# Performance work log

Measured on AMD Instinct MI355X. Metric: run time of the kernel, lower is better.

The kernel has to match this reference:

```python
import jax, jax.numpy as jnp
import numpy as np

EPS = 1e-4  # epsilon init kwarg


def setup_inputs() -> dict:
    key = jax.random.key(0)
    a = jax.random.normal(key, (8192, 64, 64), dtype=jnp.float32)
    # module assumes symmetric input (tf.self_adjoint_eig)
    x = 0.5 * (a + a.transpose(0, 2, 1))
    return {"x": x}


def reference(x):
    # batched symmetric eigendecomposition
    s, u = jnp.linalg.eigh(x)            # s: [b, d], u: [b, d, d]
    s = jnp.maximum(s, EPS)              # eigenvalue ReLU with shift epsilon
    # reconstruct: u @ diag(s) @ u^T
    return jnp.einsum('bik,bk,bjk->bij', u, s, u)
```

## Files before the change

### kernel.cpp

```cpp
#include <hip/hip_runtime.h>
#include <cstdint>


#define EPSV 1e-4f

typedef short bf16x8  __attribute__((ext_vector_type(8)));
typedef short short4v __attribute__((ext_vector_type(4)));
typedef float f32x16  __attribute__((ext_vector_type(16)));

__device__ __forceinline__ short f2bf(float f) {
  unsigned u = __float_as_uint(f);
  return (short)((u + 0x7FFFu + ((u >> 16) & 1u)) >> 16);
}
__device__ __forceinline__ float bf2f(short s) {
  return __uint_as_float(((unsigned)(unsigned short)s) << 16);
}
__device__ __forceinline__ int swz(int row, int byte) { return byte ^ ((row & 7) << 4); }
__device__ __forceinline__ void fence() { __asm volatile("" ::: "memory"); }

struct Frags { bf16x8 f[2][4]; };

__device__ __forceinline__ void loadFrags(const short* buf, int l31, int h, Frags& F) {
  #pragma unroll
  for (int mi = 0; mi < 2; mi++)
    #pragma unroll
    for (int ks = 0; ks < 4; ks++) {
      const int row = 32 * mi + l31;
      F.f[mi][ks] = *(const bf16x8*)((const char*)buf + swz(row, row * 128 + 32 * ks + 16 * h));
    }
}

__device__ __forceinline__ void chains3(const Frags& Ah, const Frags& Al,
                                        const Frags& Bh, const Frags& Bl,
                                        f32x16 acc[2][2]) {
  #pragma unroll
  for (int mi = 0; mi < 2; mi++)
    #pragma unroll
    for (int ni = 0; ni < 2; ni++)
      #pragma unroll
      for (int e = 0; e < 16; e++) acc[mi][ni][e] = 0.f;
#define MM(A, B) acc[mi][ni] = __builtin_amdgcn_mfma_f32_32x32x16_bf16(A, B, acc[mi][ni], 0, 0, 0)
  #pragma unroll
  for (int ks = 0; ks < 4; ks++) {
    #pragma unroll
    for (int mi = 0; mi < 2; mi++)
      #pragma unroll
      for (int ni = 0; ni < 2; ni++) MM(Ah.f[mi][ks], Bh.f[ni][ks]);
    #pragma unroll
    for (int mi = 0; mi < 2; mi++)
      #pragma unroll
      for (int ni = 0; ni < 2; ni++) MM(Ah.f[mi][ks], Bl.f[ni][ks]);
    #pragma unroll
    for (int mi = 0; mi < 2; mi++)
      #pragma unroll
      for (int ni = 0; ni < 2; ni++) MM(Al.f[mi][ks], Bh.f[ni][ks]);
  }
#undef MM
}

__device__ __forceinline__ void writeCT(short* bh, short* bl, const f32x16 acc[2][2],
                                        int l31, int h, float scale) {
  #pragma unroll
  for (int mi = 0; mi < 2; mi++)
    #pragma unroll
    for (int ni = 0; ni < 2; ni++) {
      const int R = 32 * ni + l31;
      #pragma unroll
      for (int q = 0; q < 4; q++) {
        short4v hv, lv;
        #pragma unroll
        for (int p = 0; p < 4; p++) {
          float v = acc[mi][ni][4 * q + p] * scale;
          short hh = f2bf(v);
          hv[p] = hh;
          lv[p] = f2bf(v - bf2f(hh));
        }
        const int off = swz(R, R * 128 + (32 * mi + 8 * q + 4 * h) * 2);
        *(short4v*)((char*)bh + off) = hv;
        *(short4v*)((char*)bl + off) = lv;
      }
    }
}

__global__ __launch_bounds__(256, 1) void mrelu_w(const float* __restrict__ X,
                                                  float* __restrict__ O, int nmat) {
  __shared__ short lds[4][16384];
  const int t = threadIdx.x, wid = t >> 6, l = t & 63;
  const int l31 = l & 31, h = l >> 5;
  const int mat = blockIdx.x * 4 + wid;
  if (mat >= nmat) return;
  const float* Xb = X + (size_t)mat * 4096;
  short* Yh = &lds[wid][0];
  short* Yl = Yh + 4096;
  short* Zh = Yh + 8192;
  short* Zl = Yh + 12288;

  float4 xv[16];
  float ssq = 0.f;
  #pragma unroll
  for (int q = 0; q < 16; q++) {
    float4 v = reinterpret_cast<const float4*>(Xb)[l + 64 * q];
    const int e = 4 * l + 256 * q, row = e >> 6, col = e & 63, d = row - col;
    if (d >= 0 && d < 4) (&v.x)[d] -= EPSV;
    ssq += v.x * v.x + v.y * v.y + v.z * v.z + v.w * v.w;
    xv[q] = v;
  }
  #pragma unroll
  for (int o = 32; o >= 1; o >>= 1) ssq += __shfl_xor(ssq, o, 64);
  const float S0 = sqrtf(ssq) + 1e-30f;
  const float invS0 = 1.0f / S0;

  #pragma unroll
  for (int q = 0; q < 16; q++) {
    const int e = 4 * l + 256 * q, row = e >> 6, col = e & 63;
    short4v hv, lv;
    #pragma unroll
    for (int i = 0; i < 4; i++) {
      float v = (&xv[q].x)[i] * invS0;
      short hh = f2bf(v);
      hv[i] = hh;
      lv[i] = f2bf(v - bf2f(hh));
    }
    const int off = swz(row, row * 128 + col * 2);
    *(short4v*)((char*)Yh + off) = hv;
    *(short4v*)((char*)Yl + off) = lv;
  }
  fence();

  Frags FA, FB, FC, FD;
  f32x16 accA[2][2], accB[2][2];

  loadFrags(Yh, l31, h, FA);
  loadFrags(Yl, l31, h, FB);
  chains3(FA, FB, FA, FB, accA);
  float zss = 0.f;
  #pragma unroll
  for (int mi = 0; mi < 2; mi++)
    #pragma unroll
    for (int ni = 0; ni < 2; ni++)
      #pragma unroll
      for (int e = 0; e < 16; e++) zss += accA[mi][ni][e] * accA[mi][ni][e];
  #pragma unroll
  for (int o = 32; o >= 1; o >>= 1) zss += __shfl_xor(zss, o, 64);
  const float rr = sqrtf(sqrtf(zss + 1e-30f));
  float lam = 1.0f / rr;
  const float lam2 = lam * lam;
  #pragma unroll
  for (int mi = 0; mi < 2; mi++)
    #pragma unroll
    for (int ni = 0; ni < 2; ni++)
      #pragma unroll
      for (int e = 0; e < 16; e++) accA[mi][ni][e] *= lam2;
  writeCT(Zh, Zl, accA, l31, h, 1.0f);
  fence();

  const float qa = 3.4445f, qb = -4.7750f, qc = 2.0315f;

  #pragma unroll 1
  for (int it = 0; it < 4; it++) {
    if (it > 0) {
      loadFrags(Yh, l31, h, FA);
      loadFrags(Yl, l31, h, FB);
      chains3(FA, FB, FA, FB, accA);
      writeCT(Zh, Zl, accA, l31, h, 1.0f);
      fence();
    }
    loadFrags(Zh, l31, h, FC);
    loadFrags(Zl, l31, h, FD);
    chains3(FC, FD, FC, FD, accB);
    #pragma unroll
    for (int mi = 0; mi < 2; mi++)
      #pragma unroll
      for (int ni = 0; ni < 2; ni++)
        #pragma unroll
        for (int r = 0; r < 16; r++) {
          const int grow = 32 * mi + (r & 3) + 8 * (r >> 2) + 4 * h;
          const int gcol = 32 * ni + l31;
          accB[mi][ni][r] = qc * accB[mi][ni][r] + qb * accA[mi][ni][r] +
                            ((grow == gcol) ? qa : 0.f);
        }
    writeCT(Zh, Zl, accB, l31, h, 1.0f);
    fence();
    loadFrags(Yh, l31, h, FA);
    loadFrags(Yl, l31, h, FB);
    loadFrags(Zh, l31, h, FC);
    loadFrags(Zl, l31, h, FD);
    chains3(FA, FB, FC, FD, accA);
    writeCT(Yh, Yl, accA, l31, h, lam);
    lam = 1.0f;
    fence();
  }

  #pragma unroll 1
  for (int it = 0; it < 3; it++) {
    loadFrags(Yh, l31, h, FA);
    loadFrags(Yl, l31, h, FB);
    chains3(FA, FB, FA, FB, accA);
    #pragma unroll
    for (int mi = 0; mi < 2; mi++)
      #pragma unroll
      for (int ni = 0; ni < 2; ni++)
        #pragma unroll
        for (int r = 0; r < 16; r++) {
          const int grow = 32 * mi + (r & 3) + 8 * (r >> 2) + 4 * h;
          const int gcol = 32 * ni + l31;
          accA[mi][ni][r] = ((grow == gcol) ? 1.5f : 0.f) - 0.5f * accA[mi][ni][r];
        }
    writeCT(Zh, Zl, accA, l31, h, 1.0f);
    fence();
    loadFrags(Zh, l31, h, FC);
    loadFrags(Zl, l31, h, FD);
    chains3(FA, FB, FC, FD, accB);
    writeCT(Yh, Yl, accB, l31, h, 1.0f);
    fence();
  }

  loadFrags(Yh, l31, h, FA);
  loadFrags(Yl, l31, h, FB);
  #pragma unroll
  for (int mi = 0; mi < 2; mi++)
    #pragma unroll
    for (int ks = 0; ks < 4; ks++) {
      const int row = 32 * mi + l31;
      const int k0 = 16 * ks + 8 * h;
      float4 a = *reinterpret_cast<const float4*>(&Xb[row * 64 + k0]);
      float4 b = *reinterpret_cast<const float4*>(&Xb[row * 64 + k0 + 4]);
      bf16x8 hh, ll;
      #pragma unroll
      for (int j = 0; j < 8; j++) {
        float v = (j < 4) ? (&a.x)[j] : (&b.x)[j - 4];
        if (row == k0 + j) v -= EPSV;
        short hb = f2bf(v);
        hh[j] = hb;
        ll[j] = f2bf(v - bf2f(hb));
      }
      FC.f[mi][ks] = hh;
      FD.f[mi][ks] = ll;
    }
  chains3(FC, FD, FA, FB, accA);
  float* Ob = O + (size_t)mat * 4096;
  #pragma unroll
  for (int mi = 0; mi < 2; mi++)
    #pragma unroll
    for (int ni = 0; ni < 2; ni++) {
      const int R = 32 * ni + l31;
      #pragma unroll
      for (int q = 0; q < 4; q++) {
        const int cb = 32 * mi + 8 * q + 4 * h;
        float4 x = *reinterpret_cast<const float4*>(&Xb[R * 64 + cb]);
        float4 o;
        #pragma unroll
        for (int p = 0; p < 4; p++)
          (&o.x)[p] = 0.5f * (&x.x)[p] + 0.5f * accA[mi][ni][4 * q + p] +
                      ((R == cb + p) ? 0.5f * EPSV : 0.f);
        *reinterpret_cast<float4*>(&Ob[R * 64 + cb]) = o;
      }
    }
}

extern "C" void kernel_launch(void* const* d_in, const int* in_sizes, int n_in,
                              void* d_out, int out_size, void* d_ws, size_t ws_size,
                              hipStream_t stream) {
  const float* X = (const float*)d_in[0];
  float* O = (float*)d_out;
  const int nmat = in_sizes[0] >> 12;
  const int blocks = (nmat + 3) / 4;
  mrelu_w<<<blocks, 256, 0, stream>>>(X, O, nmat);
}
```

Baseline: 581.8 us.

## Keep matrix iterates in registers via cross-lane shuffles instead of LDS round-trips

Removes the per-wave LDS staging of the Newton-Schulz / polar iterates and instead converts MFMA accumulator layout directly into operand fragments with __shfl_xor across lane halves, relying on matrix symmetry. The quintic update now folds the previous T fragment in during conversion rather than holding a second accumulator. Launch bounds are raised to 2 blocks per CU since no shared memory is used. This trades LDS traffic and its latency for extra shuffles and higher register pressure, which may cause spills at the new occupancy target.

```diff
diff --git a/kernel.cpp b/kernel.cpp
--- a/kernel.cpp
+++ b/kernel.cpp
@@ -5,7 +5,6 @@
 #define EPSV 1e-4f
 
 typedef short bf16x8  __attribute__((ext_vector_type(8)));
-typedef short short4v __attribute__((ext_vector_type(4)));
 typedef float f32x16  __attribute__((ext_vector_type(16)));
 
 __device__ __forceinline__ short f2bf(float f) {
@@ -15,229 +14,179 @@
 __device__ __forceinline__ float bf2f(short s) {
   return __uint_as_float(((unsigned)(unsigned short)s) << 16);
 }
-__device__ __forceinline__ int swz(int row, int byte) { return byte ^ ((row & 7) << 4); }
-__device__ __forceinline__ void fence() { __asm volatile("" ::: "memory"); }
-
-struct Frags { bf16x8 f[2][4]; };
-
-__device__ __forceinline__ void loadFrags(const short* buf, int l31, int h, Frags& F) {
-  #pragma unroll
-  for (int mi = 0; mi < 2; mi++)
-    #pragma unroll
-    for (int ks = 0; ks < 4; ks++) {
-      const int row = 32 * mi + l31;
-      F.f[mi][ks] = *(const bf16x8*)((const char*)buf + swz(row, row * 128 + 32 * ks + 16 * h));
-    }
-}
-
-__device__ __forceinline__ void chains3(const Frags& Ah, const Frags& Al,
-                                        const Frags& Bh, const Frags& Bl,
-                                        f32x16 acc[2][2]) {
+
+struct FragSet { bf16x8 h[2][4]; bf16x8 l[2][4]; };
+
+__device__ __forceinline__ void mmAcc(const FragSet& A, const FragSet& B, f32x16 acc[2][2]) {
   #pragma unroll
   for (int mi = 0; mi < 2; mi++)
     #pragma unroll
     for (int ni = 0; ni < 2; ni++)
       #pragma unroll
       for (int e = 0; e < 16; e++) acc[mi][ni][e] = 0.f;
-#define MM(A, B) acc[mi][ni] = __builtin_amdgcn_mfma_f32_32x32x16_bf16(A, B, acc[mi][ni], 0, 0, 0)
+#define MM(Af, Bf) acc[mi][ni] = __builtin_amdgcn_mfma_f32_32x32x16_bf16(Af, Bf, acc[mi][ni], 0, 0, 0)
   #pragma unroll
   for (int ks = 0; ks < 4; ks++) {
     #pragma unroll
     for (int mi = 0; mi < 2; mi++)
       #pragma unroll
-      for (int ni = 0; ni < 2; ni++) MM(Ah.f[mi][ks], Bh.f[ni][ks]);
+      for (int ni = 0; ni < 2; ni++) MM(A.h[mi][ks], B.h[ni][ks]);
     #pragma unroll
     for (int mi = 0; mi < 2; mi++)
       #pragma unroll
-      for (int ni = 0; ni < 2; ni++) MM(Ah.f[mi][ks], Bl.f[ni][ks]);
+      for (int ni = 0; ni < 2; ni++) MM(A.h[mi][ks], B.l[ni][ks]);
     #pragma unroll
     for (int mi = 0; mi < 2; mi++)
       #pragma unroll
-      for (int ni = 0; ni < 2; ni++) MM(Al.f[mi][ks], Bh.f[ni][ks]);
+      for (int ni = 0; ni < 2; ni++) MM(A.l[mi][ks], B.h[ni][ks]);
   }
 #undef MM
 }
 
-__device__ __forceinline__ void writeCT(short* bh, short* bl, const f32x16 acc[2][2],
-                                        int l31, int h, float scale) {
-  #pragma unroll
-  for (int mi = 0; mi < 2; mi++)
-    #pragma unroll
-    for (int ni = 0; ni < 2; ni++) {
-      const int R = 32 * ni + l31;
-      #pragma unroll
-      for (int q = 0; q < 4; q++) {
-        short4v hv, lv;
+template <bool ADDZ>
+__device__ __forceinline__ void convSplit(const f32x16 acc[2][2], float scale, float diag,
+                                          const FragSet* Zadd, float zc,
+                                          int l31, int h, FragSet& out) {
+  #pragma unroll
+  for (int mi = 0; mi < 2; mi++)
+    #pragma unroll
+    for (int ni = 0; ni < 2; ni++)
+      #pragma unroll
+      for (int ksp = 0; ksp < 2; ksp++) {
+        const int ks = 2 * mi + ksp;
+        const int row = 32 * ni + l31;
+        const int col0 = 16 * ks + 8 * h;
+        float v[8];
         #pragma unroll
         for (int p = 0; p < 4; p++) {
-          float v = acc[mi][ni][4 * q + p] * scale;
-          short hh = f2bf(v);
-          hv[p] = hh;
-          lv[p] = f2bf(v - bf2f(hh));
+          float a_lo = acc[mi][ni][8 * ksp + p];
+          float a_hi = acc[mi][ni][8 * ksp + 4 + p];
+          float sendv = h ? a_lo : a_hi;
+          float recv = __shfl_xor(sendv, 32, 64);
+          v[p]     = h ? recv : a_lo;
+          v[4 + p] = h ? a_hi : recv;
         }
-        const int off = swz(R, R * 128 + (32 * mi + 8 * q + 4 * h) * 2);
-        *(short4v*)((char*)bh + off) = hv;
-        *(short4v*)((char*)bl + off) = lv;
-      }
-    }
-}
-
-__global__ __launch_bounds__(256, 1) void mrelu_w(const float* __restrict__ X,
+        bf16x8 fh, fl;
+        #pragma unroll
+        for (int j = 0; j < 8; j++) {
+          float w = v[j] * scale + ((row == col0 + j) ? diag : 0.f);
+          if (ADDZ) w += zc * (bf2f(Zadd->h[ni][ks][j]) + bf2f(Zadd->l[ni][ks][j]));
+          short hh = f2bf(w);
+          fh[j] = hh;
+          fl[j] = f2bf(w - bf2f(hh));
+        }
+        out.h[ni][ks] = fh;
+        out.l[ni][ks] = fl;
+      }
+}
+
+__global__ __launch_bounds__(256, 2) void mrelu_r(const float* __restrict__ X,
                                                   float* __restrict__ O, int nmat) {
-  __shared__ short lds[4][16384];
   const int t = threadIdx.x, wid = t >> 6, l = t & 63;
   const int l31 = l & 31, h = l >> 5;
   const int mat = blockIdx.x * 4 + wid;
   if (mat >= nmat) return;
   const float* Xb = X + (size_t)mat * 4096;
-  short* Yh = &lds[wid][0];
-  short* Yl = Yh + 4096;
-  short* Zh = Yh + 8192;
-  short* Zl = Yh + 12288;
-
-  float4 xv[16];
+
+  FragSet Y, T;
+  f32x16 acc[2][2];
+
+  float xv[2][4][8];
   float ssq = 0.f;
   #pragma unroll
-  for (int q = 0; q < 16; q++) {
-    float4 v = reinterpret_cast<const float4*>(Xb)[l + 64 * q];
-    const int e = 4 * l + 256 * q, row = e >> 6, col = e & 63, d = row - col;
-    if (d >= 0 && d < 4) (&v.x)[d] -= EPSV;
-    ssq += v.x * v.x + v.y * v.y + v.z * v.z + v.w * v.w;
-    xv[q] = v;
-  }
+  for (int mi = 0; mi < 2; mi++)
+    #pragma unroll
+    for (int ks = 0; ks < 4; ks++) {
+      const int row = 32 * mi + l31;
+      const int col0 = 16 * ks + 8 * h;
+      float4 a = *reinterpret_cast<const float4*>(&Xb[row * 64 + col0]);
+      float4 b = *reinterpret_cast<const float4*>(&Xb[row * 64 + col0 + 4]);
+      #pragma unroll
+      for (int j = 0; j < 8; j++) {
+        float v = (j < 4) ? (&a.x)[j] : (&b.x)[j - 4];
+        if (row == col0 + j) v -= EPSV;
+        xv[mi][ks][j] = v;
+        ssq += v * v;
+      }
+    }
   #pragma unroll
   for (int o = 32; o >= 1; o >>= 1) ssq += __shfl_xor(ssq, o, 64);
-  const float S0 = sqrtf(ssq) + 1e-30f;
-  const float invS0 = 1.0f / S0;
-
-  #pragma unroll
-  for (int q = 0; q < 16; q++) {
-    const int e = 4 * l + 256 * q, row = e >> 6, col = e & 63;
-    short4v hv, lv;
-    #pragma unroll
-    for (int i = 0; i < 4; i++) {
-      float v = (&xv[q].x)[i] * invS0;
-      short hh = f2bf(v);
-      hv[i] = hh;
-      lv[i] = f2bf(v - bf2f(hh));
-    }
-    const int off = swz(row, row * 128 + col * 2);
-    *(short4v*)((char*)Yh + off) = hv;
-    *(short4v*)((char*)Yl + off) = lv;
-  }
-  fence();
-
-  Frags FA, FB, FC, FD;
-  f32x16 accA[2][2], accB[2][2];
-
-  loadFrags(Yh, l31, h, FA);
-  loadFrags(Yl, l31, h, FB);
-  chains3(FA, FB, FA, FB, accA);
+  const float invS0 = 1.0f / (sqrtf(ssq) + 1e-30f);
+
+  #pragma unroll
+  for (int mi = 0; mi < 2; mi++)
+    #pragma unroll
+    for (int ks = 0; ks < 4; ks++) {
+      bf16x8 fh, fl;
+      #pragma unroll
+      for (int j = 0; j < 8; j++) {
+        float v = xv[mi][ks][j] * invS0;
+        short hh = f2bf(v);
+        fh[j] = hh;
+        fl[j] = f2bf(v - bf2f(hh));
+      }
+      Y.h[mi][ks] = fh;
+      Y.l[mi][ks] = fl;
+    }
+
+  mmAcc(Y, Y, acc);
   float zss = 0.f;
   #pragma unroll
   for (int mi = 0; mi < 2; mi++)
     #pragma unroll
     for (int ni = 0; ni < 2; ni++)
       #pragma unroll
-      for (int e = 0; e < 16; e++) zss += accA[mi][ni][e] * accA[mi][ni][e];
+      for (int e = 0; e < 16; e++) zss += acc[mi][ni][e] * acc[mi][ni][e];
   #pragma unroll
   for (int o = 32; o >= 1; o >>= 1) zss += __shfl_xor(zss, o, 64);
   const float rr = sqrtf(sqrtf(zss + 1e-30f));
   float lam = 1.0f / rr;
-  const float lam2 = lam * lam;
-  #pragma unroll
-  for (int mi = 0; mi < 2; mi++)
-    #pragma unroll
-    for (int ni = 0; ni < 2; ni++)
-      #pragma unroll
-      for (int e = 0; e < 16; e++) accA[mi][ni][e] *= lam2;
-  writeCT(Zh, Zl, accA, l31, h, 1.0f);
-  fence();
+  convSplit<false>(acc, lam * lam, 0.f, nullptr, 0.f, l31, h, T);
 
   const float qa = 3.4445f, qb = -4.7750f, qc = 2.0315f;
 
   #pragma unroll 1
   for (int it = 0; it < 4; it++) {
     if (it > 0) {
-      loadFrags(Yh, l31, h, FA);
-      loadFrags(Yl, l31, h, FB);
-      chains3(FA, FB, FA, FB, accA);
-      writeCT(Zh, Zl, accA, l31, h, 1.0f);
-      fence();
-    }
-    loadFrags(Zh, l31, h, FC);
-    loadFrags(Zl, l31, h, FD);
-    chains3(FC, FD, FC, FD, accB);
-    #pragma unroll
-    for (int mi = 0; mi < 2; mi++)
-      #pragma unroll
-      for (int ni = 0; ni < 2; ni++)
-        #pragma unroll
-        for (int r = 0; r < 16; r++) {
-          const int grow = 32 * mi + (r & 3) + 8 * (r >> 2) + 4 * h;
-          const int gcol = 32 * ni + l31;
-          accB[mi][ni][r] = qc * accB[mi][ni][r] + qb * accA[mi][ni][r] +
-                            ((grow == gcol) ? qa : 0.f);
-        }
-    writeCT(Zh, Zl, accB, l31, h, 1.0f);
-    fence();
-    loadFrags(Yh, l31, h, FA);
-    loadFrags(Yl, l31, h, FB);
-    loadFrags(Zh, l31, h, FC);
-    loadFrags(Zl, l31, h, FD);
-    chains3(FA, FB, FC, FD, accA);
-    writeCT(Yh, Yl, accA, l31, h, lam);
+      mmAcc(Y, Y, acc);
+      convSplit<false>(acc, 1.f, 0.f, nullptr, 0.f, l31, h, T);
+    }
+    mmAcc(T, T, acc);
+    convSplit<true>(acc, qc, qa, &T, qb, l31, h, T);
+    mmAcc(Y, T, acc);
+    convSplit<false>(acc, lam, 0.f, nullptr, 0.f, l31, h, Y);
     lam = 1.0f;
-    fence();
   }
 
   #pragma unroll 1
   for (int it = 0; it < 3; it++) {
-    loadFrags(Yh, l31, h, FA);
-    loadFrags(Yl, l31, h, FB);
-    chains3(FA, FB, FA, FB, accA);
-    #pragma unroll
-    for (int mi = 0; mi < 2; mi++)
-      #pragma unroll
-      for (int ni = 0; ni < 2; ni++)
-        #pragma unroll
-        for (int r = 0; r < 16; r++) {
-          const int grow = 32 * mi + (r & 3) + 8 * (r >> 2) + 4 * h;
-          const int gcol = 32 * ni + l31;
-          accA[mi][ni][r] = ((grow == gcol) ? 1.5f : 0.f) - 0.5f * accA[mi][ni][r];
-        }
-    writeCT(Zh, Zl, accA, l31, h, 1.0f);
-    fence();
-    loadFrags(Zh, l31, h, FC);
-    loadFrags(Zl, l31, h, FD);
-    chains3(FA, FB, FC, FD, accB);
-    writeCT(Yh, Yl, accB, l31, h, 1.0f);
-    fence();
+    mmAcc(Y, Y, acc);
+    convSplit<false>(acc, -0.5f, 1.5f, nullptr, 0.f, l31, h, T);
+    mmAcc(Y, T, acc);
+    convSplit<false>(acc, 1.f, 0.f, nullptr, 0.f, l31, h, Y);
   }
 
-  loadFrags(Yh, l31, h, FA);
-  loadFrags(Yl, l31, h, FB);
   #pragma unroll
   for (int mi = 0; mi < 2; mi++)
     #pragma unroll
     for (int ks = 0; ks < 4; ks++) {
       const int row = 32 * mi + l31;
-      const int k0 = 16 * ks + 8 * h;
-      float4 a = *reinterpret_cast<const float4*>(&Xb[row * 64 + k0]);
-      float4 b = *reinterpret_cast<const float4*>(&Xb[row * 64 + k0 + 4]);
-      bf16x8 hh, ll;
+      const int col0 = 16 * ks + 8 * h;
+      float4 a = *reinterpret_cast<const float4*>(&Xb[row * 64 + col0]);
+      float4 b = *reinterpret_cast<const float4*>(&Xb[row * 64 + col0 + 4]);
+      bf16x8 fh, fl;
       #pragma unroll
       for (int j = 0; j < 8; j++) {
         float v = (j < 4) ? (&a.x)[j] : (&b.x)[j - 4];
-        if (row == k0 + j) v -= EPSV;
-        short hb = f2bf(v);
-        hh[j] = hb;
-        ll[j] = f2bf(v - bf2f(hb));
-      }
-      FC.f[mi][ks] = hh;
-      FD.f[mi][ks] = ll;
-    }
-  chains3(FC, FD, FA, FB, accA);
+        if (row == col0 + j) v -= EPSV;
+        short hh = f2bf(v);
+        fh[j] = hh;
+        fl[j] = f2bf(v - bf2f(hh));
+      }
+      T.h[mi][ks] = fh;
+      T.l[mi][ks] = fl;
+    }
+  mmAcc(T, Y, acc);
   float* Ob = O + (size_t)mat * 4096;
   #pragma unroll
   for (int mi = 0; mi < 2; mi++)
@@ -251,7 +200,7 @@
         float4 o;
         #pragma unroll
         for (int p = 0; p < 4; p++)
-          (&o.x)[p] = 0.5f * (&x.x)[p] + 0.5f * accA[mi][ni][4 * q + p] +
+          (&o.x)[p] = 0.5f * (&x.x)[p] + 0.5f * acc[mi][ni][4 * q + p] +
                       ((R == cb + p) ? 0.5f * EPSV : 0.f);
         *reinterpret_cast<float4*>(&Ob[R * 64 + cb]) = o;
       }
@@ -265,5 +214,5 @@
   float* O = (float*)d_out;
   const int nmat = in_sizes[0] >> 12;
   const int blocks = (nmat + 3) / 4;
-  mrelu_w<<<blocks, 256, 0, stream>>>(X, O, nmat);
-}
+  mrelu_r<<<blocks, 256, 0, stream>>>(X, O, nmat);
+}
```

Result: faster. 481.2 us (-17.3%).
